# Performance work log

Measured on AMD Instinct MI355X. Metric: run time of the kernel, lower is better.

The kernel has to match this reference:

```python
import jax, jax.numpy as jnp
import numpy as np

B, T, C, NH, L, V = 4, 1024, 768, 12, 4, 512
HD = C // NH
EPS = 1e-5


def setup_inputs() -> dict:
    key = jax.random.key(0)
    ks = jax.random.split(key, 16)
    std = 0.02
    n = lambda k, shape: jax.random.normal(k, shape, jnp.float32) * std
    return {
        "idx": jax.random.randint(ks[0], (B, T), 0, V),
        "tok_emb": n(ks[1], (V, C)),
        "type_emb": n(ks[2], (2, C)),
        "pos_emb": n(ks[3], (1, T, C)),
        "ln1_s": jnp.ones((L, C)), "ln1_b": jnp.zeros((L, C)),
        "ln2_s": jnp.ones((L, C)), "ln2_b": jnp.zeros((L, C)),
        "wq": n(ks[4], (L, C, C)), "bq": jnp.zeros((L, C)),
        "wk": n(ks[5], (L, C, C)), "bk": jnp.zeros((L, C)),
        "wv": n(ks[6], (L, C, C)), "bv": jnp.zeros((L, C)),
        "wp": n(ks[7], (L, C, C)), "bp": jnp.zeros((L, C)),
        "w1": n(ks[8], (L, C, 4 * C)), "b1": jnp.zeros((L, 4 * C)),
        "w2": n(ks[9], (L, 4 * C, C)), "b2": jnp.zeros((L, C)),
        "lnf_s": jnp.ones((C,)), "lnf_b": jnp.zeros((C,)),
        "head_w": n(ks[10], (C, V)),
    }


def _ln(x, s, b):
    m = jnp.mean(x, axis=-1, keepdims=True)
    v = jnp.mean((x - m) ** 2, axis=-1, keepdims=True)
    return (x - m) * jax.lax.rsqrt(v + EPS) * s + b


def _forward(idx, tok_emb, type_emb, pos_emb, ln1_s, ln1_b, ln2_s, ln2_b,
             wq, bq, wk, bk, wv, bv, wp, bp, w1, b1, w2, b2, lnf_s, lnf_b, head_w):
    t = idx.shape[1]
    # token + position + type(=1) embeddings; dropout is identity in eval mode
    x = tok_emb[idx] + pos_emb[:, :t, :] + type_emb[1]
    causal = jnp.tril(jnp.ones((t, t), dtype=bool))  # [T,T]
    scale = 1.0 / np.sqrt(HD)
    attn_maps = []
    for l in range(L):
        h = _ln(x, ln1_s[l], ln1_b[l])
        # project and split heads -> [B,NH,T,HD]
        def heads(w, bb):
            return (h @ w + bb).reshape(B, t, NH, HD).transpose(0, 2, 1, 3)
        q, k, v = heads(wq[l], bq[l]), heads(wk[l], bk[l]), heads(wv[l], bv[l])
        att = jnp.einsum('bhqd,bhkd->bhqk', q, k) * scale
        att = jnp.where(causal, att, -jnp.inf)
        att = jax.nn.softmax(att, axis=-1)
        attn_maps.append(att)
        y = jnp.einsum('bhqk,bhkd->bhqd', att, v)
        y = y.transpose(0, 2, 1, 3).reshape(B, t, C)
        x = x + (y @ wp[l] + bp[l])
        h2 = _ln(x, ln2_s[l], ln2_b[l])
        x = x + (jax.nn.gelu(h2 @ w1[l] + b1[l], approximate=False) @ w2[l] + b2[l])
    x = _ln(x, lnf_s, lnf_b)
    logits = x @ head_w  # head has no bias
    return logits, jnp.stack(attn_maps, axis=0)  # [L,B,NH,T,T]


def reference(idx, tok_emb, type_emb, pos_emb, ln1_s, ln1_b, ln2_s, ln2_b,
              wq, bq, wk, bk, wv, bv, wp, bp, w1, b1, w2, b2, lnf_s, lnf_b, head_w):
    return _forward(idx, tok_emb, type_emb, pos_emb, ln1_s, ln1_b, ln2_s, ln2_b,
                    wq, bq, wk, bk, wv, bv, wp, bp, w1, b1, w2, b2, lnf_s, lnf_b, head_w)
```

## Files before the change

### kernel.cpp

```cpp
#include <hip/hip_runtime.h>
#include <cstdint>


#define B_ 4
#define T_ 1024
#define C_ 768
#define NH_ 12
#define HD_ 64
#define L_ 4
#define V_ 512
#define C4_ 3072

typedef unsigned short u16;
typedef float f32x4 __attribute__((ext_vector_type(4)));
typedef short s16x8 __attribute__((ext_vector_type(8)));
typedef u16 u16x4 __attribute__((ext_vector_type(4)));
typedef u16 u16x8 __attribute__((ext_vector_type(8)));

__device__ __forceinline__ u16 f2b(float f){
  union { float f; unsigned u; } v; v.f = f;
  unsigned u = v.u + 0x7fffu + ((v.u >> 16) & 1u);
  return (u16)(u >> 16);
}

__device__ __forceinline__ float b2f(u16 b){
  return __uint_as_float(((unsigned)b) << 16);
}

__device__ __forceinline__ unsigned cvtpk(float lo, float hi){
  unsigned r;
  asm("v_cvt_pk_bf16_f32 %0, %1, %2" : "=v"(r) : "v"(lo), "v"(hi));
  return r;
}

__device__ __forceinline__ f32x4 mfma16(s16x8 a, s16x8 b, f32x4 c){
  return __builtin_amdgcn_mfma_f32_16x16x32_bf16(a, b, c, 0, 0, 0);
}

__device__ __forceinline__ void gload16(const void* g, void* l){
  __builtin_amdgcn_global_load_lds((const __attribute__((address_space(1))) unsigned*)g,
                                   (__attribute__((address_space(3))) unsigned*)l, 16, 0, 0);
}

__global__ __launch_bounds__(256) void embed_ln_kernel(const int* __restrict__ idx,
    const float* __restrict__ tok, const float* __restrict__ pos, const float* __restrict__ typ,
    const float* __restrict__ g, const float* __restrict__ bta,
    u16* __restrict__ x, u16* __restrict__ out){
  int lane = threadIdx.x & 63;
  int w = threadIdx.x >> 6;
  int row = blockIdx.x*4 + w;
  int t = row & (T_-1);
  int tk = idx[row];
  const float* tr = tok + (size_t)tk*C_;
  const float* pr = pos + (size_t)t*C_;
  float4 v[3];
  float s = 0.f;
  #pragma unroll
  for (int j=0;j<3;j++){
    int c = j*256 + lane*4;
    float4 a = *(const float4*)(tr + c);
    float4 p = *(const float4*)(pr + c);
    float4 ty = *(const float4*)(typ + c);
    v[j] = (float4){a.x+p.x+ty.x, a.y+p.y+ty.y, a.z+p.z+ty.z, a.w+p.w+ty.w};
    s += v[j].x + v[j].y + v[j].z + v[j].w;
  }
  #pragma unroll
  for (int o=32;o>0;o>>=1) s += __shfl_xor(s, o, 64);
  float mean = s * (1.0f/C_);
  float var = 0.f;
  #pragma unroll
  for (int j=0;j<3;j++){
    float dx=v[j].x-mean, dy=v[j].y-mean, dz=v[j].z-mean, dw=v[j].w-mean;
    var += dx*dx+dy*dy+dz*dz+dw*dw;
  }
  #pragma unroll
  for (int o=32;o>0;o>>=1) var += __shfl_xor(var, o, 64);
  float rs = rsqrtf(var*(1.0f/C_) + 1e-5f);
  u16* xr = x + (size_t)row*C_;
  u16* orow = out + (size_t)row*C_;
  #pragma unroll
  for (int j=0;j<3;j++){
    int c = j*256 + lane*4;
    u16x4 xv = { f2b(v[j].x), f2b(v[j].y), f2b(v[j].z), f2b(v[j].w) };
    *(u16x4*)(xr + c) = xv;
    float4 gg = *(const float4*)(g + c);
    float4 bb = *(const float4*)(bta + c);
    u16x4 o = { f2b((v[j].x-mean)*rs*gg.x + bb.x), f2b((v[j].y-mean)*rs*gg.y + bb.y),
                f2b((v[j].z-mean)*rs*gg.z + bb.z), f2b((v[j].w-mean)*rs*gg.w + bb.w) };
    *(u16x4*)(orow + c) = o;
  }
}

__global__ __launch_bounds__(256) void ln_kernel(const u16* __restrict__ x,
    const float* __restrict__ g, const float* __restrict__ bta, u16* __restrict__ out){
  int lane = threadIdx.x & 63;
  int row = blockIdx.x*4 + (threadIdx.x >> 6);
  const u16* xr = x + (size_t)row*C_;
  float v[12];
  float s = 0.f;
  #pragma unroll
  for (int j=0;j<3;j++){
    int c = j*256 + lane*4;
    u16x4 xv = *(const u16x4*)(xr + c);
    #pragma unroll
    for (int e=0;e<4;e++){ v[j*4+e] = b2f(xv[e]); s += v[j*4+e]; }
  }
  #pragma unroll
  for (int o=32;o>0;o>>=1) s += __shfl_xor(s, o, 64);
  float mean = s * (1.0f/C_);
  float var = 0.f;
  #pragma unroll
  for (int j=0;j<12;j++){ float d = v[j]-mean; var += d*d; }
  #pragma unroll
  for (int o=32;o>0;o>>=1) var += __shfl_xor(var, o, 64);
  float rs = rsqrtf(var*(1.0f/C_) + 1e-5f);
  u16* orow = out + (size_t)row*C_;
  #pragma unroll
  for (int j=0;j<3;j++){
    int c = j*256 + lane*4;
    float4 gg = *(const float4*)(g + c);
    float4 bb = *(const float4*)(bta + c);
    u16x4 o = { f2b((v[j*4+0]-mean)*rs*gg.x + bb.x), f2b((v[j*4+1]-mean)*rs*gg.y + bb.y),
                f2b((v[j*4+2]-mean)*rs*gg.z + bb.z), f2b((v[j*4+3]-mean)*rs*gg.w + bb.w) };
    *(u16x4*)(orow + c) = o;
  }
}

struct ConvTable {
  const float* src[7];
  u16* dst[7];
  int K[7], N[7], nTN[7], perZ[7];
  unsigned long long outStride[7];
  int start[8];
};

__global__ __launch_bounds__(256) void convT_all(ConvTable tab){
  int bid = blockIdx.x;
  int d = 0;
  #pragma unroll
  for (int j=1;j<7;j++) if (bid >= tab.start[j]) d = j;
  const float* src = nullptr; u16* dst = nullptr;
  int K=0, N=0, nTN=0, perZ=0; size_t oS=0;
  #pragma unroll
  for (int j=0;j<7;j++) if (d==j){ src=tab.src[j]; dst=tab.dst[j]; K=tab.K[j]; N=tab.N[j];
                                   nTN=tab.nTN[j]; perZ=tab.perZ[j]; oS=(size_t)tab.outStride[j]; }
  int local = bid - tab.start[d];
  int z = local / perZ;
  int rem = local - z*perZ;
  int tk = rem / nTN;
  int tn = rem - tk*nTN;
  int k0 = tk*64, n0 = tn*64;
  size_t inBase = (size_t)z * K * N;
  size_t outBase = (size_t)z * oS;

  __shared__ u16 t[64][68];
  #pragma unroll
  for (int rep=0;rep<4;rep++){
    int id = threadIdx.x + rep*256;
    int kr = id >> 4;
    int nc = (id & 15)*4;
    float4 v = *(const float4*)(src + inBase + (size_t)(k0+kr)*N + n0+nc);
    t[nc+0][kr] = f2b(v.x);
    t[nc+1][kr] = f2b(v.y);
    t[nc+2][kr] = f2b(v.z);
    t[nc+3][kr] = f2b(v.w);
  }
  __syncthreads();
  #pragma unroll
  for (int rep=0;rep<4;rep++){
    int id = threadIdx.x + rep*256;
    int nr = id >> 4;
    int kc = (id & 15)*4;
    u16x4 o = {t[nr][kc], t[nr][kc+1], t[nr][kc+2], t[nr][kc+3]};
    *(u16x4*)(dst + outBase + (size_t)(n0+nr)*K + k0+kc) = o;
  }
}

template<int BM, int MODE, bool GELU>
__global__ __launch_bounds__(256) void gemm_kernel(
    const u16* __restrict__ A, const u16* __restrict__ Bt,
    const float* __restrict__ bias, const float* __restrict__ bias2, const float* __restrict__ bias3,
    u16* __restrict__ outb, u16* __restrict__ outk, u16* __restrict__ outv,
    float* __restrict__ outf, u16* __restrict__ outx, int N, int K)
{
  constexpr int MT = BM/32;
  constexpr int BUF = (BM+128)*64;
  __shared__ u16 smem[2*BUF];
  const int tid = threadIdx.x;
  const int lane = tid & 63;
  const int w = tid >> 6;
  const int wm = w >> 1, wn = w & 1;

  const int gx = gridDim.x;
  const int nwg = gx * gridDim.y;
  int flat = blockIdx.y*gx + blockIdx.x;
  int swzb = (flat & 7)*(nwg >> 3) + (flat >> 3);
  const int m0 = (swzb / gx) * BM;
  const int n0 = (swzb % gx) * 128;

  const int cl = lane & 15, gr = lane >> 4;
  const int rsub = lane >> 3;
  const int swl = ((lane & 7) ^ rsub) * 8;

  f32x4 acc[MT][4];
  #pragma unroll
  for (int a=0;a<MT;a++)
    #pragma unroll
    for (int b=0;b<4;b++) acc[a][b] = (f32x4){0.f,0.f,0.f,0.f};

  auto stage = [&](int kk, u16* buf){
    u16* la = buf;
    u16* lb = buf + BM*64;
    #pragma unroll
    for (int j=0;j<MT;j++){
      int rowb = w*(BM/4) + j*8;
      gload16(A + (size_t)(m0+rowb+rsub)*K + kk + swl, &la[rowb*64]);
    }
    #pragma unroll
    for (int j=0;j<4;j++){
      int rowb = w*32 + j*8;
      gload16(Bt + (size_t)(n0+rowb+rsub)*K + kk + swl, &lb[rowb*64]);
    }
  };

  const int nSteps = K >> 6;
  stage(0, smem);

  for (int t=0; t<nSteps; t++){
    u16* cur = smem + (t&1)*BUF;
    u16* nxt = smem + ((t+1)&1)*BUF;
    if (t+1 < nSteps){
      stage((t+1)<<6, nxt);
      if constexpr (BM==128) asm volatile("s_waitcnt vmcnt(8)" ::: "memory");
      else                   asm volatile("s_waitcnt vmcnt(6)" ::: "memory");
    } else {
      asm volatile("s_waitcnt vmcnt(0)" ::: "memory");
    }
    __builtin_amdgcn_sched_barrier(0);
    __builtin_amdgcn_s_barrier();

    u16* la = cur;
    u16* lb = cur + BM*64;
    #pragma unroll
    for (int cc=0;cc<2;cc++){
      int ko = cc*32 + gr*8;
      s16x8 af[MT], bf[4];
      #pragma unroll
      for (int mt=0;mt<MT;mt++){
        int row = wm*(BM/2) + mt*16 + cl;
        af[mt] = *(const s16x8*)&la[row*64 + (ko ^ ((row&7)*8))];
      }
      #pragma unroll
      for (int nt=0;nt<4;nt++){
        int row = wn*64 + nt*16 + cl;
        bf[nt] = *(const s16x8*)&lb[row*64 + (ko ^ ((row&7)*8))];
      }
      #pragma unroll
      for (int mt=0;mt<MT;mt++)
        #pragma unroll
        for (int nt=0;nt<4;nt++)
          acc[mt][nt] = mfma16(af[mt], bf[nt], acc[mt][nt]);
    }
    __builtin_amdgcn_sched_barrier(0);
    __builtin_amdgcn_s_barrier();
  }

  if (MODE == 5){
    const int which = n0 / C_;
    const float* bp = (which==0) ? bias : (which==1) ? bias2 : bias3;
    const int nb = n0 - which*C_;
    #pragma unroll
    for (int mt=0;mt<MT;mt++){
      #pragma unroll
      for (int nt=0;nt<4;nt++){
        #pragma unroll
        for (int i=0;i<4;i++){
          int tl = wm*(BM/2) + mt*16 + gr*4 + i;
          int dl = wn*64 + nt*16 + cl;
          smem[tl*128 + (dl ^ ((tl&7)*8))] = f2b(acc[mt][nt][i] + bp[nb + dl]);
        }
      }
    }
    __syncthreads();
    const int b = m0 >> 10, tg = m0 & (T_-1);
    if (which < 2){
      u16* outp = which ? outk : outb;
      constexpr int TPR = 256/BM;
      constexpr int CPT = 16/TPR;
      int r = tid / TPR;
      int sub = tid % TPR;
      #pragma unroll
      for (int j=0;j<CPT;j++){
        int ch = sub*CPT + j;
        int h = (nb >> 6) + (ch >> 3);
        int dd = (ch & 7)*8;
        u16x8 vv = *(const u16x8*)&smem[r*128 + ((ch ^ (r&7))*8)];
        *(u16x8*)&outp[(((size_t)b*NH_ + h)*T_ + tg + r)*HD_ + dd] = vv;
      }
    } else {
      constexpr int TCH = BM/16;
      int r = tid >> 1;
      int half = tid & 1;
      int dg = nb + r;
      int h = dg >> 6, dd = dg & (HD_-1);
      u16* orow = outv + (((size_t)b*NH_ + h)*HD_ + dd)*T_ + tg;
      #pragma unroll
      for (int j=0;j<TCH;j++){
        int t0 = half*(BM/2) + j*8;
        u16x8 vv;
        #pragma unroll
        for (int s2=0;s2<8;s2++){
          int t = t0 + s2;
          vv[s2] = smem[t*128 + (r ^ ((t&7)*8))];
        }
        *(u16x8*)&orow[t0] = vv;
      }
    }
  } else if (MODE == 0){
    #pragma unroll
    for (int mt=0;mt<MT;mt++){
      #pragma unroll
      for (int nt=0;nt<4;nt++){
        #pragma unroll
        for (int i=0;i<4;i++){
          int tl = wm*(BM/2) + mt*16 + gr*4 + i;
          int dl = wn*64 + nt*16 + cl;
          float val = acc[mt][nt][i] + bias[n0 + dl];
          if (GELU) val = 0.5f*val*(1.0f + erff(val*0.70710678118654752440f));
          smem[tl*128 + (dl ^ ((tl&7)*8))] = f2b(val);
        }
      }
    }
    __syncthreads();
    constexpr int TPR = 256/BM;
    constexpr int CPT = 16/TPR;
    int r = tid / TPR;
    int sub = tid % TPR;
    u16* orow = outb + (size_t)(m0 + r)*N + n0;
    #pragma unroll
    for (int j=0;j<CPT;j++){
      int ch = sub*CPT + j;
      u16x8 vv = *(const u16x8*)&smem[r*128 + ((ch ^ (r&7))*8)];
      *(u16x8*)&orow[ch*8] = vv;
    }
  } else if (MODE == 3){
    static_assert(BM == 64, "MODE 3 fp32 restage sized for BM=64");
    float* lds_f = (float*)smem;
    #pragma unroll
    for (int mt=0;mt<MT;mt++){
      #pragma unroll
      for (int nt=0;nt<4;nt++){
        #pragma unroll
        for (int i=0;i<4;i++){
          int tl = wm*(BM/2) + mt*16 + gr*4 + i;
          int dl = wn*64 + nt*16 + cl;
          float val = acc[mt][nt][i];
          if (bias) val += bias[n0 + dl];
          lds_f[tl*132 + dl] = val;
        }
      }
    }
    __syncthreads();
    constexpr int TPR = 256/BM;
    constexpr int CPT = 16/TPR;
    int r = tid / TPR;
    int sub = tid % TPR;
    u16* xrow = outx + (size_t)(m0 + r)*N + n0;
    #pragma unroll
    for (int j=0;j<CPT;j++){
      int ch = sub*CPT + j;
      u16x8 xv = *(const u16x8*)&xrow[ch*8];
      const float* lf = &lds_f[r*132 + ch*8];
      u16x8 ov;
      #pragma unroll
      for (int e=0;e<8;e++) ov[e] = f2b(b2f(xv[e]) + lf[e]);
      *(u16x8*)&xrow[ch*8] = ov;
    }
  } else {
    #pragma unroll
    for (int mt=0;mt<MT;mt++){
      #pragma unroll
      for (int nt=0;nt<4;nt++){
        #pragma unroll
        for (int i=0;i<4;i++){
          int gm = m0 + wm*(BM/2) + mt*16 + gr*4 + i;
          int gn = n0 + wn*64 + nt*16 + cl;
          float val = acc[mt][nt][i];
          if (bias) val += bias[gn];
          outf[(size_t)gm*N + gn] = val;
        }
      }
    }
  }
}

__global__ __launch_bounds__(256,2) void attn_kernel(
    const u16* __restrict__ q, const u16* __restrict__ k, const u16* __restrict__ vt,
    float* __restrict__ att, u16* __restrict__ y, int layer)
{
  __shared__ u16 pl[4][16*64];
  const int lane = threadIdx.x & 63;
  const int w = threadIdx.x >> 6;
  const int qt = 15 - blockIdx.x;
  const int bh = blockIdx.y;
  const int bb = bh / NH_;
  const int hh = bh - bb*NH_;
  const int q0 = qt*64 + w*16;
  const u16* qbase = q + (size_t)bh*T_*HD_;
  const u16* kbase = k + (size_t)bh*T_*HD_;
  const u16* vbase = vt + (size_t)bh*HD_*T_;
  float* abase = att + ((size_t)layer*B_*NH_ + bh)*((size_t)T_*T_);
  u16* plw = &pl[w][0];

  const int cl = lane & 15, gr = lane >> 4;
  const int d0 = gr*8;
  const int swz = (cl & 7)*8;
  const int myq = q0 + cl;

  s16x8 qf0 = *(const s16x8*)(qbase + (size_t)(q0+cl)*HD_ + d0);
  s16x8 qf1 = *(const s16x8*)(qbase + (size_t)(q0+cl)*HD_ + 32 + d0);

  const float scale = 0.125f;
  const int nkt = qt + 1;

  unsigned pbuf[16][8];
  float slocal = 0.f;
  f32x4 yacc[4];
  #pragma unroll
  for (int n=0;n<4;n++) yacc[n] = (f32x4){0.f,0.f,0.f,0.f};

  #pragma unroll
  for (int kt=0; kt<16; kt++){
    if (kt < nkt){
      #pragma unroll
      for (int n=0;n<4;n++){
        int krow = kt*64 + n*16 + cl;
        s16x8 kf0 = *(const s16x8*)(kbase + (size_t)krow*HD_ + d0);
        s16x8 kf1 = *(const s16x8*)(kbase + (size_t)krow*HD_ + 32 + d0);
        f32x4 dacc = (f32x4){0.f,0.f,0.f,0.f};
        dacc = mfma16(kf0, qf0, dacc);
        dacc = mfma16(kf1, qf1, dacc);
        float p[4];
        #pragma unroll
        for (int i=0;i<4;i++){
          float sv = dacc[i]*scale;
          int kk = kt*64 + n*16 + gr*4 + i;
          if (kt == qt && kk > myq) sv = -1e30f;
          p[i] = __expf(sv);
        }
        slocal += (p[0]+p[1]) + (p[2]+p[3]);
        unsigned lo = cvtpk(p[0],p[1]), hi = cvtpk(p[2],p[3]);
        pbuf[kt][2*n]   = lo;
        pbuf[kt][2*n+1] = hi;
        int colb = (n*16 + gr*4) ^ swz;
        *(uint2*)&plw[cl*64 + colb] = make_uint2(lo, hi);
      }
      asm volatile("s_waitcnt lgkmcnt(0)" ::: "memory");
      __builtin_amdgcn_sched_barrier(0);
      #pragma unroll
      for (int cc=0;cc<2;cc++){
        s16x8 pa = *(const s16x8*)&plw[cl*64 + ((cc*32 + d0) ^ swz)];
        #pragma unroll
        for (int n2=0;n2<4;n2++){
          s16x8 bv = *(const s16x8*)(vbase + (size_t)(n2*16+cl)*T_ + kt*64 + cc*32 + d0);
          yacc[n2] = mfma16(pa, bv, yacc[n2]);
        }
      }
    }
  }

  slocal += __shfl_xor(slocal, 16, 64);
  slocal += __shfl_xor(slocal, 32, 64);
  float inv = 1.0f / slocal;

  float invy[4];
  #pragma unroll
  for (int i=0;i<4;i++) invy[i] = __shfl(inv, gr*4 + i, 64);

  #pragma unroll
  for (int n2=0;n2<4;n2++){
    #pragma unroll
    for (int i=0;i<4;i++){
      int r = q0 + gr*4 + i;
      y[((size_t)bb*T_ + r)*C_ + hh*HD_ + n2*16 + cl] = f2b(yacc[n2][i]*invy[i]);
    }
  }

  #pragma unroll
  for (int kt=0; kt<16; kt++){
    if (kt < nkt){
      #pragma unroll
      for (int n=0;n<4;n++){
        unsigned lo = pbuf[kt][2*n], hi = pbuf[kt][2*n+1];
        float p0 = __uint_as_float(lo << 16)          * inv;
        float p1 = __uint_as_float(lo & 0xffff0000u)  * inv;
        float p2 = __uint_as_float(hi << 16)          * inv;
        float p3 = __uint_as_float(hi & 0xffff0000u)  * inv;
        *(float4*)&abase[(size_t)myq*T_ + kt*64 + n*16 + gr*4] = make_float4(p0,p1,p2,p3);
      }
    }
  }

  int kend = nkt*64;
  if (kend < T_){
    int w4 = (T_ - kend) >> 2;
    for (int r = w; r < 64; r += 4){
      float* rp = abase + (size_t)(qt*64 + r)*T_ + kend;
      for (int c = lane; c < w4; c += 64){
        *(float4*)(rp + c*4) = make_float4(0.f,0.f,0.f,0.f);
      }
    }
  }
}

extern "C" void kernel_launch(void* const* d_in, const int* in_sizes, int n_in,
                              void* d_out, int out_size, void* d_ws, size_t ws_size,
                              hipStream_t stream)
{
  (void)in_sizes; (void)n_in; (void)out_size; (void)ws_size;
  const int*   idx  = (const int*)d_in[0];
  const float* tok  = (const float*)d_in[1];
  const float* typ  = (const float*)d_in[2];
  const float* pos  = (const float*)d_in[3];
  const float* ln1s = (const float*)d_in[4];
  const float* ln1b = (const float*)d_in[5];
  const float* ln2s = (const float*)d_in[6];
  const float* ln2b = (const float*)d_in[7];
  const float* wq   = (const float*)d_in[8];
  const float* bq   = (const float*)d_in[9];
  const float* wk   = (const float*)d_in[10];
  const float* bk   = (const float*)d_in[11];
  const float* wv   = (const float*)d_in[12];
  const float* bv   = (const float*)d_in[13];
  const float* wp   = (const float*)d_in[14];
  const float* bp   = (const float*)d_in[15];
  const float* w1   = (const float*)d_in[16];
  const float* b1   = (const float*)d_in[17];
  const float* w2   = (const float*)d_in[18];
  const float* b2   = (const float*)d_in[19];
  const float* lnfs = (const float*)d_in[20];
  const float* lnfb = (const float*)d_in[21];
  const float* hw   = (const float*)d_in[22];

  char* ws = (char*)d_ws;
  u16* x      = (u16*)(ws + 0);
  u16* hbf    = (u16*)(ws + 12582912);
  u16* qb     = (u16*)(ws + 18874368);
  u16* kb     = (u16*)(ws + 25165824);
  u16* vtb    = (u16*)(ws + 31457280);
  u16* yb     = (u16*)(ws + 37748736);
  u16* h2     = (u16*)(ws + 44040192);
  u16* wqkvT  = (u16*)(ws + 69206016);
  u16* wpT    = (u16*)(ws + 83361792);
  u16* w1T    = (u16*)(ws + 88080384);
  u16* w2T    = (u16*)(ws + 106954752);
  u16* hwT    = (u16*)(ws + 125829120);

  float* logits = (float*)d_out;
  float* att = logits + (size_t)B_*T_*V_;

  const size_t CC   = (size_t)C_*C_;
  const size_t CC4  = (size_t)C_*C4_;
  const size_t QKVL = (size_t)3*C_*C_;

  ConvTable tab;
  const float* srcs[7] = {wq, wk, wv, wp, w1, w2, hw};
  u16* dsts[7] = {wqkvT, wqkvT + CC, wqkvT + 2*CC, wpT, w1T, w2T, hwT};
  int Ks[7]   = {C_, C_, C_, C_, C_,  C4_, C_};
  int Ns[7]   = {C_, C_, C_, C_, C4_, C_,  V_};
  int nzs[7]  = {L_, L_, L_, L_, L_,  L_,  1};
  unsigned long long oss[7] = {QKVL, QKVL, QKVL, CC, CC4, CC4, CC};
  int acc = 0;
  for (int j=0;j<7;j++){
    tab.src[j]=srcs[j]; tab.dst[j]=dsts[j]; tab.K[j]=Ks[j]; tab.N[j]=Ns[j];
    tab.nTN[j]=Ns[j]/64; tab.perZ[j]=(Ks[j]/64)*(Ns[j]/64); tab.outStride[j]=oss[j];
    tab.start[j]=acc; acc += tab.perZ[j]*nzs[j];
  }
  tab.start[7]=acc;
  convT_all<<<acc, 256, 0, stream>>>(tab);

  embed_ln_kernel<<<1024, 256, 0, stream>>>(idx, tok, pos, typ + C_, ln1s, ln1b, x, hbf);

  for (int l=0; l<L_; l++){
    if (l > 0)
      ln_kernel<<<1024, 256, 0, stream>>>(x, ln1s + l*C_, ln1b + l*C_, hbf);
    gemm_kernel<64,5,false><<<dim3(18,64), 256, 0, stream>>>(
        hbf, wqkvT + l*QKVL, bq + l*C_, bk + l*C_, bv + l*C_,
        qb, kb, vtb, nullptr, nullptr, 3*C_, C_);
    attn_kernel<<<dim3(16,48), 256, 0, stream>>>(qb, kb, vtb, att, yb, l);
    gemm_kernel<64,3,false><<<dim3(6,64), 256, 0, stream>>>(
        yb, wpT + l*CC, bp + l*C_, nullptr, nullptr,
        nullptr, nullptr, nullptr, nullptr, x, C_, C_);
    ln_kernel<<<1024, 256, 0, stream>>>(x, ln2s + l*C_, ln2b + l*C_, hbf);
    gemm_kernel<64,0,true><<<dim3(24,64), 256, 0, stream>>>(
        hbf, w1T + l*CC4, b1 + l*C4_, nullptr, nullptr,
        h2, nullptr, nullptr, nullptr, nullptr, C4_, C_);
    gemm_kernel<64,3,false><<<dim3(6,64), 256, 0, stream>>>(
        h2, w2T + l*CC4, b2 + l*C_, nullptr, nullptr,
        nullptr, nullptr, nullptr, nullptr, x, C_, C4_);
  }
  ln_kernel<<<1024, 256, 0, stream>>>(x, lnfs, lnfb, hbf);
  gemm_kernel<64,4,false><<<dim3(4,64), 256, 0, stream>>>(
      hbf, hwT, nullptr, nullptr, nullptr,
      nullptr, nullptr, nullptr, logits, nullptr, V_, C_);
}
```

Baseline: 1.040 ms.

## Fold LayerNorm into GEMM epilogues via row stats and precomputed weight column sums

Removes all standalone LayerNorm kernels. The gamma scale is folded into the bf16 transposed weights, and column sums of the scaled weights plus beta-weighted column sums are accumulated atomically during the weight conversion. Residual-add epilogues and the embedding kernel accumulate per-row sum and sum of squares with atomics. Consuming GEMMs then apply mean/rstd algebraically on the raw residual stream. This saves a full read/write pass per LN and several launches, but adds atomics, a memset, and numerical risk from the E[x^2]-mean^2 variance and from rounding gamma-scaled weights to bf16.

```diff
diff --git a/kernel.cpp b/kernel.cpp
--- a/kernel.cpp
+++ b/kernel.cpp
@@ -42,10 +42,9 @@
                                    (__attribute__((address_space(3))) unsigned*)l, 16, 0, 0);
 }
 
-__global__ __launch_bounds__(256) void embed_ln_kernel(const int* __restrict__ idx,
+__global__ __launch_bounds__(256) void embed_kernel(const int* __restrict__ idx,
     const float* __restrict__ tok, const float* __restrict__ pos, const float* __restrict__ typ,
-    const float* __restrict__ g, const float* __restrict__ bta,
-    u16* __restrict__ x, u16* __restrict__ out){
+    u16* __restrict__ x, float* __restrict__ statsOut){
   int lane = threadIdx.x & 63;
   int w = threadIdx.x >> 6;
   int row = blockIdx.x*4 + w;
@@ -54,7 +53,8 @@
   const float* tr = tok + (size_t)tk*C_;
   const float* pr = pos + (size_t)t*C_;
   float4 v[3];
-  float s = 0.f;
+  float s = 0.f, sq = 0.f;
+  u16* xr = x + (size_t)row*C_;
   #pragma unroll
   for (int j=0;j<3;j++){
     int c = j*256 + lane*4;
@@ -62,75 +62,30 @@
     float4 p = *(const float4*)(pr + c);
     float4 ty = *(const float4*)(typ + c);
     v[j] = (float4){a.x+p.x+ty.x, a.y+p.y+ty.y, a.z+p.z+ty.z, a.w+p.w+ty.w};
-    s += v[j].x + v[j].y + v[j].z + v[j].w;
-  }
-  #pragma unroll
-  for (int o=32;o>0;o>>=1) s += __shfl_xor(s, o, 64);
-  float mean = s * (1.0f/C_);
-  float var = 0.f;
-  #pragma unroll
-  for (int j=0;j<3;j++){
-    float dx=v[j].x-mean, dy=v[j].y-mean, dz=v[j].z-mean, dw=v[j].w-mean;
-    var += dx*dx+dy*dy+dz*dz+dw*dw;
-  }
-  #pragma unroll
-  for (int o=32;o>0;o>>=1) var += __shfl_xor(var, o, 64);
-  float rs = rsqrtf(var*(1.0f/C_) + 1e-5f);
-  u16* xr = x + (size_t)row*C_;
-  u16* orow = out + (size_t)row*C_;
-  #pragma unroll
-  for (int j=0;j<3;j++){
-    int c = j*256 + lane*4;
     u16x4 xv = { f2b(v[j].x), f2b(v[j].y), f2b(v[j].z), f2b(v[j].w) };
     *(u16x4*)(xr + c) = xv;
-    float4 gg = *(const float4*)(g + c);
-    float4 bb = *(const float4*)(bta + c);
-    u16x4 o = { f2b((v[j].x-mean)*rs*gg.x + bb.x), f2b((v[j].y-mean)*rs*gg.y + bb.y),
-                f2b((v[j].z-mean)*rs*gg.z + bb.z), f2b((v[j].w-mean)*rs*gg.w + bb.w) };
-    *(u16x4*)(orow + c) = o;
-  }
-}
-
-__global__ __launch_bounds__(256) void ln_kernel(const u16* __restrict__ x,
-    const float* __restrict__ g, const float* __restrict__ bta, u16* __restrict__ out){
-  int lane = threadIdx.x & 63;
-  int row = blockIdx.x*4 + (threadIdx.x >> 6);
-  const u16* xr = x + (size_t)row*C_;
-  float v[12];
-  float s = 0.f;
-  #pragma unroll
-  for (int j=0;j<3;j++){
-    int c = j*256 + lane*4;
-    u16x4 xv = *(const u16x4*)(xr + c);
-    #pragma unroll
-    for (int e=0;e<4;e++){ v[j*4+e] = b2f(xv[e]); s += v[j*4+e]; }
-  }
-  #pragma unroll
-  for (int o=32;o>0;o>>=1) s += __shfl_xor(s, o, 64);
-  float mean = s * (1.0f/C_);
-  float var = 0.f;
-  #pragma unroll
-  for (int j=0;j<12;j++){ float d = v[j]-mean; var += d*d; }
-  #pragma unroll
-  for (int o=32;o>0;o>>=1) var += __shfl_xor(var, o, 64);
-  float rs = rsqrtf(var*(1.0f/C_) + 1e-5f);
-  u16* orow = out + (size_t)row*C_;
-  #pragma unroll
-  for (int j=0;j<3;j++){
-    int c = j*256 + lane*4;
-    float4 gg = *(const float4*)(g + c);
-    float4 bb = *(const float4*)(bta + c);
-    u16x4 o = { f2b((v[j*4+0]-mean)*rs*gg.x + bb.x), f2b((v[j*4+1]-mean)*rs*gg.y + bb.y),
-                f2b((v[j*4+2]-mean)*rs*gg.z + bb.z), f2b((v[j*4+3]-mean)*rs*gg.w + bb.w) };
-    *(u16x4*)(orow + c) = o;
+    float e0=b2f(xv[0]), e1=b2f(xv[1]), e2=b2f(xv[2]), e3=b2f(xv[3]);
+    s  += e0+e1+e2+e3;
+    sq += e0*e0+e1*e1+e2*e2+e3*e3;
+  }
+  #pragma unroll
+  for (int o=32;o>0;o>>=1){ s += __shfl_xor(s, o, 64); sq += __shfl_xor(sq, o, 64); }
+  if (lane == 0){
+    statsOut[2*row]   = s;
+    statsOut[2*row+1] = sq;
   }
 }
 
 struct ConvTable {
   const float* src[7];
   u16* dst[7];
+  const float* gam[7];
+  const float* bet[7];
+  float* sOut[7];
+  float* cOut[7];
   int K[7], N[7], nTN[7], perZ[7];
   unsigned long long outStride[7];
+  int sZs[7], sCol[7];
   int start[8];
 };
 
@@ -140,10 +95,16 @@
   #pragma unroll
   for (int j=1;j<7;j++) if (bid >= tab.start[j]) d = j;
   const float* src = nullptr; u16* dst = nullptr;
-  int K=0, N=0, nTN=0, perZ=0; size_t oS=0;
-  #pragma unroll
-  for (int j=0;j<7;j++) if (d==j){ src=tab.src[j]; dst=tab.dst[j]; K=tab.K[j]; N=tab.N[j];
-                                   nTN=tab.nTN[j]; perZ=tab.perZ[j]; oS=(size_t)tab.outStride[j]; }
+  const float* gamB = nullptr; const float* betB = nullptr;
+  float* sOutB = nullptr; float* cOutB = nullptr;
+  int K=0, N=0, nTN=0, perZ=0, sZs=0, sCol=0; size_t oS=0;
+  #pragma unroll
+  for (int j=0;j<7;j++) if (d==j){
+    src=tab.src[j]; dst=tab.dst[j]; gamB=tab.gam[j]; betB=tab.bet[j];
+    sOutB=tab.sOut[j]; cOutB=tab.cOut[j];
+    K=tab.K[j]; N=tab.N[j]; nTN=tab.nTN[j]; perZ=tab.perZ[j];
+    oS=(size_t)tab.outStride[j]; sZs=tab.sZs[j]; sCol=tab.sCol[j];
+  }
   int local = bid - tab.start[d];
   int z = local / perZ;
   int rem = local - z*perZ;
@@ -152,18 +113,40 @@
   int k0 = tk*64, n0 = tn*64;
   size_t inBase = (size_t)z * K * N;
   size_t outBase = (size_t)z * oS;
+  const float* gamp = gamB ? gamB + (size_t)z*C_ : nullptr;
+  const float* betp = betB ? betB + (size_t)z*C_ : nullptr;
+  float* sB = sOutB ? sOutB + (size_t)z*sZs + sCol : nullptr;
+  float* cB = cOutB ? cOutB + (size_t)z*sZs + sCol : nullptr;
 
   __shared__ u16 t[64][68];
+  float sacc[4] = {0.f,0.f,0.f,0.f};
+  float cacc[4] = {0.f,0.f,0.f,0.f};
+  int nc_fixed = (threadIdx.x & 15)*4;
   #pragma unroll
   for (int rep=0;rep<4;rep++){
     int id = threadIdx.x + rep*256;
     int kr = id >> 4;
     int nc = (id & 15)*4;
-    float4 v = *(const float4*)(src + inBase + (size_t)(k0+kr)*N + n0+nc);
-    t[nc+0][kr] = f2b(v.x);
-    t[nc+1][kr] = f2b(v.y);
-    t[nc+2][kr] = f2b(v.z);
-    t[nc+3][kr] = f2b(v.w);
+    int k = k0 + kr;
+    float4 v = *(const float4*)(src + inBase + (size_t)k*N + n0+nc);
+    float gv = gamp ? gamp[k] : 1.f;
+    float bv = betp ? betp[k] : 0.f;
+    float s0=v.x*gv, s1=v.y*gv, s2=v.z*gv, s3=v.w*gv;
+    t[nc+0][kr] = f2b(s0);
+    t[nc+1][kr] = f2b(s1);
+    t[nc+2][kr] = f2b(s2);
+    t[nc+3][kr] = f2b(s3);
+    if (sB){
+      sacc[0]+=s0; sacc[1]+=s1; sacc[2]+=s2; sacc[3]+=s3;
+      cacc[0]+=bv*v.x; cacc[1]+=bv*v.y; cacc[2]+=bv*v.z; cacc[3]+=bv*v.w;
+    }
+  }
+  if (sB){
+    #pragma unroll
+    for (int e=0;e<4;e++){
+      atomicAdd(&sB[n0 + nc_fixed + e], sacc[e]);
+      atomicAdd(&cB[n0 + nc_fixed + e], cacc[e]);
+    }
   }
   __syncthreads();
   #pragma unroll
@@ -181,7 +164,10 @@
     const u16* __restrict__ A, const u16* __restrict__ Bt,
     const float* __restrict__ bias, const float* __restrict__ bias2, const float* __restrict__ bias3,
     u16* __restrict__ outb, u16* __restrict__ outk, u16* __restrict__ outv,
-    float* __restrict__ outf, u16* __restrict__ outx, int N, int K)
+    float* __restrict__ outf, u16* __restrict__ outx,
+    const float* __restrict__ colS, const float* __restrict__ colC,
+    const float* __restrict__ rowStats, float* __restrict__ statsOut,
+    int N, int K)
 {
   constexpr int MT = BM/32;
   constexpr int BUF = (BM+128)*64;
@@ -265,10 +251,34 @@
     __builtin_amdgcn_s_barrier();
   }
 
+  float meanv[MT][4], rsv[MT][4];
+  if (MODE == 0 || MODE == 4 || MODE == 5){
+    #pragma unroll
+    for (int mt=0;mt<MT;mt++){
+      #pragma unroll
+      for (int i=0;i<4;i++){
+        int grow = m0 + wm*(BM/2) + mt*16 + gr*4 + i;
+        float S1 = rowStats[2*grow], S2 = rowStats[2*grow+1];
+        float m = S1 * (1.0f/C_);
+        float vv = S2 * (1.0f/C_) - m*m;
+        meanv[mt][i] = m;
+        rsv[mt][i] = rsqrtf(vv + 1e-5f);
+      }
+    }
+  }
+
   if (MODE == 5){
     const int which = n0 / C_;
     const float* bp = (which==0) ? bias : (which==1) ? bias2 : bias3;
     const int nb = n0 - which*C_;
+    float sv4[4], cv4[4], bb4[4];
+    #pragma unroll
+    for (int nt=0;nt<4;nt++){
+      int gn = n0 + wn*64 + nt*16 + cl;
+      sv4[nt] = colS[gn];
+      cv4[nt] = colC[gn];
+      bb4[nt] = bp[nb + wn*64 + nt*16 + cl];
+    }
     #pragma unroll
     for (int mt=0;mt<MT;mt++){
       #pragma unroll
@@ -277,7 +287,9 @@
         for (int i=0;i<4;i++){
           int tl = wm*(BM/2) + mt*16 + gr*4 + i;
           int dl = wn*64 + nt*16 + cl;
-          smem[tl*128 + (dl ^ ((tl&7)*8))] = f2b(acc[mt][nt][i] + bp[nb + dl]);
+          float rs = rsv[mt][i];
+          float val = rs*acc[mt][nt][i] - rs*meanv[mt][i]*sv4[nt] + cv4[nt] + bb4[nt];
+          smem[tl*128 + (dl ^ ((tl&7)*8))] = f2b(val);
         }
       }
     }
@@ -317,6 +329,14 @@
       }
     }
   } else if (MODE == 0){
+    float sv4[4], cv4[4], bb4[4];
+    #pragma unroll
+    for (int nt=0;nt<4;nt++){
+      int gn = n0 + wn*64 + nt*16 + cl;
+      sv4[nt] = colS[gn];
+      cv4[nt] = colC[gn];
+      bb4[nt] = bias[gn];
+    }
     #pragma unroll
     for (int mt=0;mt<MT;mt++){
       #pragma unroll
@@ -325,7 +345,8 @@
         for (int i=0;i<4;i++){
           int tl = wm*(BM/2) + mt*16 + gr*4 + i;
           int dl = wn*64 + nt*16 + cl;
-          float val = acc[mt][nt][i] + bias[n0 + dl];
+          float rs = rsv[mt][i];
+          float val = rs*acc[mt][nt][i] - rs*meanv[mt][i]*sv4[nt] + cv4[nt] + bb4[nt];
           if (GELU) val = 0.5f*val*(1.0f + erff(val*0.70710678118654752440f));
           smem[tl*128 + (dl ^ ((tl&7)*8))] = f2b(val);
         }
@@ -366,6 +387,7 @@
     int r = tid / TPR;
     int sub = tid % TPR;
     u16* xrow = outx + (size_t)(m0 + r)*N + n0;
+    float S1p = 0.f, S2p = 0.f;
     #pragma unroll
     for (int j=0;j<CPT;j++){
       int ch = sub*CPT + j;
@@ -373,10 +395,25 @@
       const float* lf = &lds_f[r*132 + ch*8];
       u16x8 ov;
       #pragma unroll
-      for (int e=0;e<8;e++) ov[e] = f2b(b2f(xv[e]) + lf[e]);
+      for (int e=0;e<8;e++){
+        u16 nb_ = f2b(b2f(xv[e]) + lf[e]);
+        ov[e] = nb_;
+        float nv = b2f(nb_);
+        S1p += nv;
+        S2p += nv*nv;
+      }
       *(u16x8*)&xrow[ch*8] = ov;
     }
+    atomicAdd(&statsOut[2*(m0 + r)],     S1p);
+    atomicAdd(&statsOut[2*(m0 + r) + 1], S2p);
   } else {
+    float sv4[4], cv4[4];
+    #pragma unroll
+    for (int nt=0;nt<4;nt++){
+      int gn = n0 + wn*64 + nt*16 + cl;
+      sv4[nt] = colS[gn];
+      cv4[nt] = colC[gn];
+    }
     #pragma unroll
     for (int mt=0;mt<MT;mt++){
       #pragma unroll
@@ -385,8 +422,8 @@
         for (int i=0;i<4;i++){
           int gm = m0 + wm*(BM/2) + mt*16 + gr*4 + i;
           int gn = n0 + wn*64 + nt*16 + cl;
-          float val = acc[mt][nt][i];
-          if (bias) val += bias[gn];
+          float rs = rsv[mt][i];
+          float val = rs*acc[mt][nt][i] - rs*meanv[mt][i]*sv4[nt] + cv4[nt];
           outf[(size_t)gm*N + gn] = val;
         }
       }
@@ -544,7 +581,13 @@
 
   char* ws = (char*)d_ws;
   u16* x      = (u16*)(ws + 0);
-  u16* hbf    = (u16*)(ws + 12582912);
+  float* stats = (float*)(ws + 12582912);
+  float* sQ    = (float*)(ws + 12877824);
+  float* sM1   = sQ + 4*2304;
+  float* sH    = sM1 + 4*3072;
+  float* cQ    = (float*)(ws + 12965888);
+  float* cM1   = cQ + 4*2304;
+  float* cH    = cM1 + 4*3072;
   u16* qb     = (u16*)(ws + 18874368);
   u16* kb     = (u16*)(ws + 25165824);
   u16* vtb    = (u16*)(ws + 31457280);
@@ -563,44 +606,60 @@
   const size_t CC4  = (size_t)C_*C4_;
   const size_t QKVL = (size_t)3*C_*C_;
 
+  hipMemsetAsync(ws + 12582912, 0, 13053952 - 12582912, stream);
+
   ConvTable tab;
   const float* srcs[7] = {wq, wk, wv, wp, w1, w2, hw};
   u16* dsts[7] = {wqkvT, wqkvT + CC, wqkvT + 2*CC, wpT, w1T, w2T, hwT};
+  const float* gams[7] = {ln1s, ln1s, ln1s, nullptr, ln2s, nullptr, lnfs};
+  const float* bets[7] = {ln1b, ln1b, ln1b, nullptr, ln2b, nullptr, lnfb};
+  float* sOuts[7] = {sQ, sQ, sQ, nullptr, sM1, nullptr, sH};
+  float* cOuts[7] = {cQ, cQ, cQ, nullptr, cM1, nullptr, cH};
+  int sZss[7]  = {2304, 2304, 2304, 0, 3072, 0, 0};
+  int sCols[7] = {0, 768, 1536, 0, 0, 0, 0};
   int Ks[7]   = {C_, C_, C_, C_, C_,  C4_, C_};
   int Ns[7]   = {C_, C_, C_, C_, C4_, C_,  V_};
   int nzs[7]  = {L_, L_, L_, L_, L_,  L_,  1};
   unsigned long long oss[7] = {QKVL, QKVL, QKVL, CC, CC4, CC4, CC};
   int acc = 0;
   for (int j=0;j<7;j++){
-    tab.src[j]=srcs[j]; tab.dst[j]=dsts[j]; tab.K[j]=Ks[j]; tab.N[j]=Ns[j];
+    tab.src[j]=srcs[j]; tab.dst[j]=dsts[j];
+    tab.gam[j]=gams[j]; tab.bet[j]=bets[j];
+    tab.sOut[j]=sOuts[j]; tab.cOut[j]=cOuts[j];
+    tab.K[j]=Ks[j]; tab.N[j]=Ns[j];
     tab.nTN[j]=Ns[j]/64; tab.perZ[j]=(Ks[j]/64)*(Ns[j]/64); tab.outStride[j]=oss[j];
+    tab.sZs[j]=sZss[j]; tab.sCol[j]=sCols[j];
     tab.start[j]=acc; acc += tab.perZ[j]*nzs[j];
   }
   tab.start[7]=acc;
   convT_all<<<acc, 256, 0, stream>>>(tab);
 
-  embed_ln_kernel<<<1024, 256, 0, stream>>>(idx, tok, pos, typ + C_, ln1s, ln1b, x, hbf);
+  embed_kernel<<<1024, 256, 0, stream>>>(idx, tok, pos, typ + C_, x, stats);
 
   for (int l=0; l<L_; l++){
-    if (l > 0)
-      ln_kernel<<<1024, 256, 0, stream>>>(x, ln1s + l*C_, ln1b + l*C_, hbf);
+    float* stQKV = stats + (size_t)(2*l)*8192;
+    float* stPrj = stats + (size_t)(2*l+1)*8192;
+    float* stMl2 = stats + (size_t)(2*l+2)*8192;
     gemm_kernel<64,5,false><<<dim3(18,64), 256, 0, stream>>>(
-        hbf, wqkvT + l*QKVL, bq + l*C_, bk + l*C_, bv + l*C_,
-        qb, kb, vtb, nullptr, nullptr, 3*C_, C_);
+        x, wqkvT + l*QKVL, bq + l*C_, bk + l*C_, bv + l*C_,
+        qb, kb, vtb, nullptr, nullptr,
+        sQ + l*2304, cQ + l*2304, stQKV, nullptr, 3*C_, C_);
     attn_kernel<<<dim3(16,48), 256, 0, stream>>>(qb, kb, vtb, att, yb, l);
     gemm_kernel<64,3,false><<<dim3(6,64), 256, 0, stream>>>(
         yb, wpT + l*CC, bp + l*C_, nullptr, nullptr,
-        nullptr, nullptr, nullptr, nullptr, x, C_, C_);
-    ln_kernel<<<1024, 256, 0, stream>>>(x, ln2s + l*C_, ln2b + l*C_, hbf);
+        nullptr, nullptr, nullptr, nullptr, x,
+        nullptr, nullptr, nullptr, stPrj, C_, C_);
     gemm_kernel<64,0,true><<<dim3(24,64), 256, 0, stream>>>(
-        hbf, w1T + l*CC4, b1 + l*C4_, nullptr, nullptr,
-        h2, nullptr, nullptr, nullptr, nullptr, C4_, C_);
+        x, w1T + l*CC4, b1 + l*C4_, nullptr, nullptr,
+        h2, nullptr, nullptr, nullptr, nullptr,
+        sM1 + l*3072, cM1 + l*3072, stPrj, nullptr, C4_, C_);
     gemm_kernel<64,3,false><<<dim3(6,64), 256, 0, stream>>>(
         h2, w2T + l*CC4, b2 + l*C_, nullptr, nullptr,
-        nullptr, nullptr, nullptr, nullptr, x, C_, C4_);
-  }
-  ln_kernel<<<1024, 256, 0, stream>>>(x, lnfs, lnfb, hbf);
+        nullptr, nullptr, nullptr, nullptr, x,
+        nullptr, nullptr, nullptr, stMl2, C_, C4_);
+  }
   gemm_kernel<64,4,false><<<dim3(4,64), 256, 0, stream>>>(
-      hbf, hwT, nullptr, nullptr, nullptr,
-      nullptr, nullptr, nullptr, logits, nullptr, V_, C_);
-}
+      x, hwT, nullptr, nullptr, nullptr,
+      nullptr, nullptr, nullptr, logits, nullptr,
+      sH, cH, stats + (size_t)8*8192, nullptr, V_, C_);
+}
```

Result: slower. 1.353 ms (+30.1%).
